# Optimization experiments

Hardware: AMD Instinct MI355X
Metric: run time of the kernel (lower is better)

The kernel has to match this reference:

```python
import jax, jax.numpy as jnp
import numpy as np

HASHMAPS = [(50, 32, 1.0), (200, 16, 0.5), (400, 8, 0.25), (400, 4, 0.125), (400, 3, 0.05)]
CONCAT = 63  # 32+16+8+4+3
PRIMES = jnp.array([73856093, 19349663, 83492791], dtype=jnp.int32)
# corner order idx = i*4 + j*2 + k, bit 0 -> floor, bit 1 -> ceil (matches torch loop)
BITS = jnp.array([[i, j, k] for i in range(2) for j in range(2) for k in range(2)], dtype=jnp.int32)  # (8,3)


def _encode(pos, table, vsl):
    # pos: (N,3) float32; table: (hsize, D)
    p = pos / vsl
    fl = jnp.floor(p)
    fl_i = fl.astype(jnp.int32)
    ce_i = jnp.ceil(p).astype(jnp.int32)
    sel = jnp.where(BITS[None, :, :] == 0, fl_i[:, None, :], ce_i[:, None, :])  # (N,8,3) int32
    sp = sel * PRIMES  # int32 wraparound, same as torch
    h = jnp.mod((sp[..., 0] ^ sp[..., 1]) ^ sp[..., 2], table.shape[0])  # (N,8), nonneg
    emb = table[h]  # (N,8,D) gather
    r = p - fl  # (N,3) trilinear fractions
    # faithful to original: frac weights the FLOOR-corner group (m1/m2/m3 masks)
    lin1 = r[:, 0:1, None] * emb[:, :4] + (1.0 - r[:, 0:1, None]) * emb[:, 4:]   # (N,4,D)
    lin2 = r[:, 1:2, None] * lin1[:, :2] + (1.0 - r[:, 1:2, None]) * lin1[:, 2:]  # (N,2,D)
    lin3 = r[:, 2:3] * lin2[:, 0] + (1.0 - r[:, 2:3]) * lin2[:, 1]               # (N,D)
    return lin3


def setup_inputs() -> dict:
    key = jax.random.key(0)
    ks = jax.random.split(key, 16)
    N = 262144
    inp = {"x": jax.random.normal(ks[0], (N, 3), dtype=jnp.float32)}
    for lvl, (hsize, dim, _) in enumerate(HASHMAPS):
        inp[f"emb{lvl}"] = jax.random.normal(ks[1 + lvl], (hsize, dim), dtype=jnp.float32)
    s = 1.0 / np.sqrt(CONCAT)
    inp["Wd1"] = jax.random.uniform(ks[6], (CONCAT, CONCAT), jnp.float32, -s, s)
    inp["bd1"] = jax.random.uniform(ks[7], (CONCAT,), jnp.float32, -s, s)
    inp["Wd2"] = jax.random.uniform(ks[8], (CONCAT, 1), jnp.float32, -s, s)
    inp["bd2"] = jax.random.uniform(ks[9], (1,), jnp.float32, -s, s)
    inp["Wc1"] = jax.random.uniform(ks[10], (CONCAT, CONCAT), jnp.float32, -s, s)
    inp["bc1"] = jax.random.uniform(ks[11], (CONCAT,), jnp.float32, -s, s)
    inp["Wc2"] = jax.random.uniform(ks[12], (CONCAT, 3), jnp.float32, -s, s)
    inp["bc2"] = jax.random.uniform(ks[13], (3,), jnp.float32, -s, s)
    return inp


def reference(x, emb0, emb1, emb2, emb3, emb4, Wd1, bd1, Wd2, bd2, Wc1, bc1, Wc2, bc2):
    tables = [emb0, emb1, emb2, emb3, emb4]
    feats = [_encode(x, tables[i], HASHMAPS[i][2]) for i in range(5)]
    f = jnp.concatenate(feats, axis=1)  # (N,63)
    dense = jax.nn.relu(f @ Wd1 + bd1) @ Wd2 + bd2  # (N,1)
    color = jax.nn.relu(f @ Wc1 + bc1) @ Wc2 + bc2  # (N,3)
    return (dense, color)
```

## Files before the change

### kernel.cpp

```cpp
#include <hip/hip_runtime.h>
#include <hip/hip_fp16.h>


#define NPTS 262144
#define BLOCK 1024
#define PTS_PER_BLOCK 256

#define IMG_TAB   0
#define IMG_WTF   32768
#define IMG_BW    49152
#define IMG_BYTES 51200

#define OFF_L0 0
#define OFF_L1 2000
#define OFF_L2 6000
#define OFF_L3 10800
#define OFF_L4 12400
#define TAB_HALFS 16384

typedef _Float16 f16x8 __attribute__((ext_vector_type(8)));
typedef _Float16 f16x4 __attribute__((ext_vector_type(4)));
typedef float f32x4 __attribute__((ext_vector_type(4)));

__device__ __forceinline__ void async_cp16(const void* g, void* l) {
    __builtin_amdgcn_global_load_lds(
        (__attribute__((address_space(1))) unsigned int*)const_cast<void*>(g),
        (__attribute__((address_space(3))) unsigned int*)l, 16, 0, 0);
}

__global__ void prep_kernel(const float* __restrict__ Wd1, const float* __restrict__ bd1,
                            const float* __restrict__ Wd2,
                            const float* __restrict__ Wc1, const float* __restrict__ bc1,
                            const float* __restrict__ Wc2,
                            const float* __restrict__ e0, const float* __restrict__ e1,
                            const float* __restrict__ e2, const float* __restrict__ e3,
                            const float* __restrict__ e4,
                            void* __restrict__ ws) {
    _Float16* tab = (_Float16*)((char*)ws + IMG_TAB);
    _Float16* wtf = (_Float16*)((char*)ws + IMG_WTF);
    float*    bw  = (float*)((char*)ws + IMG_BW);
    const int gtid = blockIdx.x * blockDim.x + threadIdx.x;
    const int gstr = gridDim.x * blockDim.x;

    for (int i = gtid; i < 1024; i += gstr) {
        int nt = i >> 7, rem = i & 127, s = rem >> 6, l = rem & 63;
        int kq = l >> 4, lo = l & 15, col = nt * 16 + lo;
#pragma unroll
        for (int j = 0; j < 8; ++j) {
            int k = s * 32 + kq * 8 + j;
            float v = 0.f;
            if (k < 63) {
                if (col < 63) v = Wd1[k * 63 + col];
                else if (col >= 64 && col < 127) v = Wc1[k * 63 + (col - 64)];
            }
            wtf[i * 8 + j] = (_Float16)v;
        }
    }
    for (int i = gtid; i < 512; i += gstr) {
        float v = 0.f;
        if (i < 128) {
            if (i < 63) v = bd1[i];
            else if (i >= 64 && i < 127) v = bc1[i - 64];
        } else if (i < 192) {
            int t = i - 128; v = (t < 63) ? Wd2[t] : 0.f;
        } else if (i < 448) {
            int t = i - 192, c = t >> 2, j = t & 3;
            v = (c < 63 && j < 3) ? Wc2[c * 3 + j] : 0.f;
        }
        bw[i] = v;
    }
    for (int idx = gtid; idx < 50 * 40; idx += gstr) {
        int r = idx / 40, c = idx - r * 40;
        tab[OFF_L0 + idx] = (c < 32) ? (_Float16)e0[r * 32 + c] : (_Float16)0.f;
    }
    for (int idx = gtid; idx < 200 * 20; idx += gstr) {
        int r = idx / 20, c = idx - r * 20;
        tab[OFF_L1 + idx] = (c < 16) ? (_Float16)e1[r * 16 + c] : (_Float16)0.f;
    }
    for (int idx = gtid; idx < 400 * 12; idx += gstr) {
        int r = idx / 12, c = idx - r * 12;
        tab[OFF_L2 + idx] = (c < 8) ? (_Float16)e2[r * 8 + c] : (_Float16)0.f;
    }
    for (int idx = gtid; idx < 400 * 4; idx += gstr)
        tab[OFF_L3 + idx] = (_Float16)e3[idx];
    for (int idx = gtid; idx < 400 * 4; idx += gstr) {
        int r = idx >> 2, c = idx & 3;
        tab[OFF_L4 + idx] = (c < 3) ? (_Float16)e4[r * 3 + c] : (_Float16)0.f;
    }
    for (int idx = 14000 + gtid; idx < TAB_HALFS; idx += gstr)
        tab[idx] = (_Float16)0.f;
}

__device__ __forceinline__ int pymod(int v, int H, int sh) {
    unsigned vu = (unsigned)v ^ 0x80000000u;
    unsigned q = __umulhi(vu >> sh, 0x51EB851Fu) >> 3;
    int m = (int)(vu - q * (unsigned)H);
    int h = m - 48;
    return h < 0 ? h + H : h;
}

struct Corner {
    int ax0, ax1, ay0, ay1, az0, az1;
    float rx, ry, rz;
};
__device__ __forceinline__ Corner mkcorner(float px, float py, float pz) {
    Corner c;
    float fx = floorf(px), fy = floorf(py), fz = floorf(pz);
    c.rx = px - fx; c.ry = py - fy; c.rz = pz - fz;
    c.ax0 = (int)((unsigned)(int)fx * 73856093u);
    c.ax1 = (int)((unsigned)(int)ceilf(px) * 73856093u);
    c.ay0 = (int)((unsigned)(int)fy * 19349663u);
    c.ay1 = (int)((unsigned)(int)ceilf(py) * 19349663u);
    c.az0 = (int)((unsigned)(int)fz * 83492791u);
    c.az1 = (int)((unsigned)(int)ceilf(pz) * 83492791u);
    return c;
}

#define CXOR(C, cc) ((((cc) & 4) ? C.ax1 : C.ax0) ^ (((cc) & 2) ? C.ay1 : C.ay0) \
                   ^ (((cc) & 1) ? C.az1 : C.az0))
#define CW(C, cc) ((((cc) & 4) ? (1.f - C.rx) : C.rx) * \
                   (((cc) & 2) ? (1.f - C.ry) : C.ry) * \
                   (((cc) & 1) ? (1.f - C.rz) : C.rz))

#define ROR_ADD(v, CTRL) { \
    int _t = __builtin_amdgcn_update_dpp(0, __float_as_int(v), (CTRL), 0xF, 0xF, true); \
    (v) += __int_as_float(_t); }
__device__ __forceinline__ float rowsum16(float v) {
    ROR_ADD(v, 0x121)
    ROR_ADD(v, 0x122)
    ROR_ADD(v, 0x124)
    ROR_ADD(v, 0x128)
    return v;
}

__global__ __launch_bounds__(BLOCK, 8) void nerf_fwd(
    const float* __restrict__ x,
    const float* __restrict__ bd2, const float* __restrict__ bc2,
    const void* __restrict__ ws,
    float* __restrict__ out)
{
    __shared__ __align__(16) char ldsb[IMG_BYTES];
    const int tid = threadIdx.x;

    {
        const char* gsrc = (const char*)ws + tid * 16;
        char* ldst = ldsb + tid * 16;
#pragma unroll
        for (int i = 0; i < 3; ++i)
            async_cp16(gsrc + i * 16384, ldst + i * 16384);
        if (tid < 128)
            async_cp16(gsrc + 3 * 16384, ldst + 3 * 16384);
    }

    const int l  = tid & 63;
    const int lo = l & 15;
    const int kq = l >> 4;
    const int wb = blockIdx.x * PTS_PER_BLOCK + (tid >> 6) * 16;
    const int p  = wb + lo;

    const float x0 = x[3 * p + 0], x1 = x[3 * p + 1], x2 = x[3 * p + 2];

    const bool q2 = (kq == 2), q3 = (kq == 3);
    const int  g  = kq >> 1;
    const int  H  = 200 << g;
    const int  sh = 3 + g;
    const float sA = q3 ? 8.f : (q2 ? 4.f : 2.f);
    const int tb0 = q3 ? OFF_L3 : (q2 ? OFF_L2 : OFF_L1);
    const int st  = q3 ? 4 : (q2 ? 12 : 20);
    const int fo0 = (kq == 1) ? 8 : 0;
    const int tb1 = q3 ? OFF_L4 : tb0;
    const int fo1 = q3 ? 0 : fo0 + 4;

    Corner ca = mkcorner(x0, x1, x2);
    Corner cb = mkcorner(x0 * sA, x1 * sA, x2 * sA);
    Corner cb1;
    {
        const float dx = x0 / 0.05f, dy = x1 / 0.05f, dz = x2 / 0.05f;
        const float b1x = q3 ? dx : x0 * sA, b1y = q3 ? dy : x1 * sA,
                    b1z = q3 ? dz : x2 * sA;
        cb1 = mkcorner(b1x, b1y, b1z);
    }
    int hA[8], h0[8], h1[8];
#pragma unroll
    for (int cc = 0; cc < 8; ++cc) hA[cc] = pymod(CXOR(ca, cc), 50, 1);
#pragma unroll
    for (int cc = 0; cc < 8; ++cc) h0[cc] = pymod(CXOR(cb, cc), H, sh);
#pragma unroll
    for (int cc = 0; cc < 8; ++cc) h1[cc] = pymod(CXOR(cb1, cc), H, sh);

    const float bd2v = bd2[0];
    const float bcx = bc2[0], bcy = bc2[1], bcz = bc2[2];

    __syncthreads();

    const _Float16* ldsT = (const _Float16*)ldsb;
    const f16x8* wtf = (const f16x8*)(ldsb + IMG_WTF);
    const float* b1c = (const float*)(ldsb + IMG_BW);
    const float* w2d = b1c + 128;
    const float4* w2c = (const float4*)(b1c + 192);

    const int kq8 = kq * 8;
    f16x8 va[8];
#pragma unroll
    for (int cc = 0; cc < 8; ++cc)
        va[cc] = *(const f16x8*)(ldsT + OFF_L0 + hA[cc] * 40 + kq8);
    f16x4 ea[8];
#pragma unroll
    for (int cc = 0; cc < 8; ++cc)
        ea[cc] = *(const f16x4*)(ldsT + tb0 + h0[cc] * st + fo0);

    float fA[8] = {0.f, 0.f, 0.f, 0.f, 0.f, 0.f, 0.f, 0.f};
#pragma unroll
    for (int cc = 0; cc < 8; ++cc) {
        float w = CW(ca, cc);
#pragma unroll
        for (int j = 0; j < 8; ++j)
            fA[j] = fmaf((float)va[cc][j], w, fA[j]);
    }

    f16x4 eb[8];
#pragma unroll
    for (int cc = 0; cc < 8; ++cc)
        eb[cc] = *(const f16x4*)(ldsT + tb1 + h1[cc] * st + fo1);

    float fB[8] = {0.f, 0.f, 0.f, 0.f, 0.f, 0.f, 0.f, 0.f};
#pragma unroll
    for (int cc = 0; cc < 8; ++cc) {
        float w = CW(cb, cc);
        fB[0] = fmaf((float)ea[cc][0], w, fB[0]); fB[1] = fmaf((float)ea[cc][1], w, fB[1]);
        fB[2] = fmaf((float)ea[cc][2], w, fB[2]); fB[3] = fmaf((float)ea[cc][3], w, fB[3]);
    }
#pragma unroll
    for (int cc = 0; cc < 8; ++cc) {
        float w = CW(cb1, cc);
        fB[4] = fmaf((float)eb[cc][0], w, fB[4]); fB[5] = fmaf((float)eb[cc][1], w, fB[5]);
        fB[6] = fmaf((float)eb[cc][2], w, fB[6]); fB[7] = fmaf((float)eb[cc][3], w, fB[7]);
    }
    if (q3) fB[7] = 0.f;

    union AF { unsigned u[4]; f16x8 h; } a0, a1;
#pragma unroll
    for (int j = 0; j < 4; ++j) {
        __half2 t0 = __floats2half2_rn(fA[2 * j], fA[2 * j + 1]);
        __half2 t1 = __floats2half2_rn(fB[2 * j], fB[2 * j + 1]);
        a0.u[j] = *(unsigned*)&t0;
        a1.u[j] = *(unsigned*)&t1;
    }

    float pd[4]  = {0.f, 0.f, 0.f, 0.f};
    float pc0[4] = {0.f, 0.f, 0.f, 0.f};
    float pc1[4] = {0.f, 0.f, 0.f, 0.f};
    float pc2[4] = {0.f, 0.f, 0.f, 0.f};

#pragma unroll
    for (int nt = 0; nt < 8; ++nt) {
        f16x8 b0 = wtf[(nt * 2 + 0) * 64 + l];
        f16x8 b1 = wtf[(nt * 2 + 1) * 64 + l];
        f32x4 c = {0.f, 0.f, 0.f, 0.f};
        c = __builtin_amdgcn_mfma_f32_16x16x32_f16(a0.h, b0, c, 0, 0, 0);
        c = __builtin_amdgcn_mfma_f32_16x16x32_f16(a1.h, b1, c, 0, 0, 0);
        float bias = b1c[nt * 16 + lo];
        if (nt < 4) {
            float w2 = w2d[nt * 16 + lo];
#pragma unroll
            for (int r = 0; r < 4; ++r)
                pd[r] = fmaf(fmaxf(c[r] + bias, 0.f), w2, pd[r]);
        } else {
            float4 wc = w2c[(nt - 4) * 16 + lo];
#pragma unroll
            for (int r = 0; r < 4; ++r) {
                float t = fmaxf(c[r] + bias, 0.f);
                pc0[r] = fmaf(t, wc.x, pc0[r]);
                pc1[r] = fmaf(t, wc.y, pc1[r]);
                pc2[r] = fmaf(t, wc.z, pc2[r]);
            }
        }
    }

#pragma unroll
    for (int r = 0; r < 4; ++r) {
        pd[r]  = rowsum16(pd[r]);
        pc0[r] = rowsum16(pc0[r]);
        pc1[r] = rowsum16(pc1[r]);
        pc2[r] = rowsum16(pc2[r]);
    }

    if (lo < 4) {
        float badd = (lo == 0) ? bd2v : ((lo == 1) ? bcx : ((lo == 2) ? bcy : bcz));
#pragma unroll
        for (int r = 0; r < 4; ++r) {
            int row = wb + kq * 4 + r;
            int addr = (lo == 0) ? row : (NPTS + row * 3 + (lo - 1));
            float v = (lo == 0) ? pd[r]
                    : ((lo == 1) ? pc0[r] : ((lo == 2) ? pc1[r] : pc2[r]));
            out[addr] = v + badd;
        }
    }
}

extern "C" void kernel_launch(void* const* d_in, const int* in_sizes, int n_in,
                              void* d_out, int out_size, void* d_ws, size_t ws_size,
                              hipStream_t stream) {
    const float* x   = (const float*)d_in[0];
    const float* e0  = (const float*)d_in[1];
    const float* e1  = (const float*)d_in[2];
    const float* e2  = (const float*)d_in[3];
    const float* e3  = (const float*)d_in[4];
    const float* e4  = (const float*)d_in[5];
    const float* Wd1 = (const float*)d_in[6];
    const float* bd1 = (const float*)d_in[7];
    const float* Wd2 = (const float*)d_in[8];
    const float* bd2 = (const float*)d_in[9];
    const float* Wc1 = (const float*)d_in[10];
    const float* bc1 = (const float*)d_in[11];
    const float* Wc2 = (const float*)d_in[12];
    const float* bc2 = (const float*)d_in[13];
    float* out = (float*)d_out;

    prep_kernel<<<64, 256, 0, stream>>>(Wd1, bd1, Wd2, Wc1, bc1, Wc2,
                                        e0, e1, e2, e3, e4, d_ws);
    nerf_fwd<<<dim3(NPTS / PTS_PER_BLOCK), dim3(BLOCK), 0, stream>>>(
        x, bd2, bc2, d_ws, out);
}
```

Measured before the change: 38.00 us.

## Shrink LDS image, halve block size, read bias/W2 from global as float4

```diff
diff --git a/kernel.cpp b/kernel.cpp
--- a/kernel.cpp
+++ b/kernel.cpp
@@ -3,24 +3,26 @@
 
 
 #define NPTS 262144
-#define BLOCK 1024
-#define PTS_PER_BLOCK 256
+#define BLOCK 512
+#define PTS_PER_BLOCK 128
 
 #define IMG_TAB   0
-#define IMG_WTF   32768
-#define IMG_BW    49152
-#define IMG_BYTES 51200
+#define IMG_WTF   24576
+#define IMG_BYTES 40960
+#define IMG_WZ    40960
 
 #define OFF_L0 0
-#define OFF_L1 2000
-#define OFF_L2 6000
-#define OFF_L3 10800
-#define OFF_L4 12400
-#define TAB_HALFS 16384
+#define OFF_L1 1600
+#define OFF_L2 4800
+#define OFF_L3 8000
+#define OFF_L4 9600
+#define TAB_HALFS 12288
 
 typedef _Float16 f16x8 __attribute__((ext_vector_type(8)));
 typedef _Float16 f16x4 __attribute__((ext_vector_type(4)));
 typedef float f32x4 __attribute__((ext_vector_type(4)));
+
+union AF { unsigned u[4]; f16x8 h; };
 
 __device__ __forceinline__ void async_cp16(const void* g, void* l) {
     __builtin_amdgcn_global_load_lds(
@@ -38,7 +40,7 @@
                             void* __restrict__ ws) {
     _Float16* tab = (_Float16*)((char*)ws + IMG_TAB);
     _Float16* wtf = (_Float16*)((char*)ws + IMG_WTF);
-    float*    bw  = (float*)((char*)ws + IMG_BW);
+    float*    bw  = (float*)((char*)ws + IMG_WZ);
     const int gtid = blockIdx.x * blockDim.x + threadIdx.x;
     const int gstr = gridDim.x * blockDim.x;
 
@@ -57,37 +59,32 @@
         }
     }
     for (int i = gtid; i < 512; i += gstr) {
+        int col = i >> 2, j = i & 3;
         float v = 0.f;
-        if (i < 128) {
-            if (i < 63) v = bd1[i];
-            else if (i >= 64 && i < 127) v = bc1[i - 64];
-        } else if (i < 192) {
-            int t = i - 128; v = (t < 63) ? Wd2[t] : 0.f;
-        } else if (i < 448) {
-            int t = i - 192, c = t >> 2, j = t & 3;
-            v = (c < 63 && j < 3) ? Wc2[c * 3 + j] : 0.f;
+        if (j == 0) {
+            if (col < 63) v = bd1[col];
+            else if (col >= 64 && col < 127) v = bc1[col - 64];
+        } else if (col < 64) {
+            if (j == 1 && col < 63) v = Wd2[col];
+        } else {
+            int c2 = col - 64;
+            if (c2 < 63) v = Wc2[c2 * 3 + (j - 1)];
         }
         bw[i] = v;
     }
-    for (int idx = gtid; idx < 50 * 40; idx += gstr) {
-        int r = idx / 40, c = idx - r * 40;
-        tab[OFF_L0 + idx] = (c < 32) ? (_Float16)e0[r * 32 + c] : (_Float16)0.f;
-    }
-    for (int idx = gtid; idx < 200 * 20; idx += gstr) {
-        int r = idx / 20, c = idx - r * 20;
-        tab[OFF_L1 + idx] = (c < 16) ? (_Float16)e1[r * 16 + c] : (_Float16)0.f;
-    }
-    for (int idx = gtid; idx < 400 * 12; idx += gstr) {
-        int r = idx / 12, c = idx - r * 12;
-        tab[OFF_L2 + idx] = (c < 8) ? (_Float16)e2[r * 8 + c] : (_Float16)0.f;
-    }
+    for (int idx = gtid; idx < 50 * 32; idx += gstr)
+        tab[OFF_L0 + idx] = (_Float16)e0[idx];
+    for (int idx = gtid; idx < 200 * 16; idx += gstr)
+        tab[OFF_L1 + idx] = (_Float16)e1[idx];
+    for (int idx = gtid; idx < 400 * 8; idx += gstr)
+        tab[OFF_L2 + idx] = (_Float16)e2[idx];
     for (int idx = gtid; idx < 400 * 4; idx += gstr)
         tab[OFF_L3 + idx] = (_Float16)e3[idx];
     for (int idx = gtid; idx < 400 * 4; idx += gstr) {
         int r = idx >> 2, c = idx & 3;
         tab[OFF_L4 + idx] = (c < 3) ? (_Float16)e4[r * 3 + c] : (_Float16)0.f;
     }
-    for (int idx = 14000 + gtid; idx < TAB_HALFS; idx += gstr)
+    for (int idx = 11200 + gtid; idx < TAB_HALFS; idx += gstr)
         tab[idx] = (_Float16)0.f;
 }
 
@@ -146,10 +143,8 @@
         const char* gsrc = (const char*)ws + tid * 16;
         char* ldst = ldsb + tid * 16;
 #pragma unroll
-        for (int i = 0; i < 3; ++i)
-            async_cp16(gsrc + i * 16384, ldst + i * 16384);
-        if (tid < 128)
-            async_cp16(gsrc + 3 * 16384, ldst + 3 * 16384);
+        for (int i = 0; i < 5; ++i)
+            async_cp16(gsrc + i * 8192, ldst + i * 8192);
     }
 
     const int l  = tid & 63;
@@ -166,7 +161,7 @@
     const int  sh = 3 + g;
     const float sA = q3 ? 8.f : (q2 ? 4.f : 2.f);
     const int tb0 = q3 ? OFF_L3 : (q2 ? OFF_L2 : OFF_L1);
-    const int st  = q3 ? 4 : (q2 ? 12 : 20);
+    const int st  = q3 ? 4 : (q2 ? 8 : 16);
     const int fo0 = (kq == 1) ? 8 : 0;
     const int tb1 = q3 ? OFF_L4 : tb0;
     const int fo1 = q3 ? 0 : fo0 + 4;
@@ -195,15 +190,13 @@
 
     const _Float16* ldsT = (const _Float16*)ldsb;
     const f16x8* wtf = (const f16x8*)(ldsb + IMG_WTF);
-    const float* b1c = (const float*)(ldsb + IMG_BW);
-    const float* w2d = b1c + 128;
-    const float4* w2c = (const float4*)(b1c + 192);
+    const float4* wz = (const float4*)((const char*)ws + IMG_WZ);
 
     const int kq8 = kq * 8;
     f16x8 va[8];
 #pragma unroll
     for (int cc = 0; cc < 8; ++cc)
-        va[cc] = *(const f16x8*)(ldsT + OFF_L0 + hA[cc] * 40 + kq8);
+        va[cc] = *(const f16x8*)(ldsT + OFF_L0 + hA[cc] * 32 + kq8);
     f16x4 ea[8];
 #pragma unroll
     for (int cc = 0; cc < 8; ++cc)
@@ -238,7 +231,7 @@
     }
     if (q3) fB[7] = 0.f;
 
-    union AF { unsigned u[4]; f16x8 h; } a0, a1;
+    AF a0, a1;
 #pragma unroll
     for (int j = 0; j < 4; ++j) {
         __half2 t0 = __floats2half2_rn(fA[2 * j], fA[2 * j + 1]);
@@ -248,9 +241,9 @@
     }
 
     float pd[4]  = {0.f, 0.f, 0.f, 0.f};
-    float pc0[4] = {0.f, 0.f, 0.f, 0.f};
-    float pc1[4] = {0.f, 0.f, 0.f, 0.f};
-    float pc2[4] = {0.f, 0.f, 0.f, 0.f};
+    float px[4]  = {0.f, 0.f, 0.f, 0.f};
+    float py[4]  = {0.f, 0.f, 0.f, 0.f};
+    float pz[4]  = {0.f, 0.f, 0.f, 0.f};
 
 #pragma unroll
     for (int nt = 0; nt < 8; ++nt) {
@@ -259,30 +252,28 @@
         f32x4 c = {0.f, 0.f, 0.f, 0.f};
         c = __builtin_amdgcn_mfma_f32_16x16x32_f16(a0.h, b0, c, 0, 0, 0);
         c = __builtin_amdgcn_mfma_f32_16x16x32_f16(a1.h, b1, c, 0, 0, 0);
-        float bias = b1c[nt * 16 + lo];
+        float4 z = wz[nt * 16 + lo];
         if (nt < 4) {
-            float w2 = w2d[nt * 16 + lo];
 #pragma unroll
             for (int r = 0; r < 4; ++r)
-                pd[r] = fmaf(fmaxf(c[r] + bias, 0.f), w2, pd[r]);
+                pd[r] = fmaf(fmaxf(c[r] + z.x, 0.f), z.y, pd[r]);
         } else {
-            float4 wc = w2c[(nt - 4) * 16 + lo];
 #pragma unroll
             for (int r = 0; r < 4; ++r) {
-                float t = fmaxf(c[r] + bias, 0.f);
-                pc0[r] = fmaf(t, wc.x, pc0[r]);
-                pc1[r] = fmaf(t, wc.y, pc1[r]);
-                pc2[r] = fmaf(t, wc.z, pc2[r]);
+                float t = fmaxf(c[r] + z.x, 0.f);
+                px[r] = fmaf(t, z.y, px[r]);
+                py[r] = fmaf(t, z.z, py[r]);
+                pz[r] = fmaf(t, z.w, pz[r]);
             }
         }
     }
 
 #pragma unroll
     for (int r = 0; r < 4; ++r) {
-        pd[r]  = rowsum16(pd[r]);
-        pc0[r] = rowsum16(pc0[r]);
-        pc1[r] = rowsum16(pc1[r]);
-        pc2[r] = rowsum16(pc2[r]);
+        pd[r] = rowsum16(pd[r]);
+        px[r] = rowsum16(px[r]);
+        py[r] = rowsum16(py[r]);
+        pz[r] = rowsum16(pz[r]);
     }
 
     if (lo < 4) {
@@ -292,7 +283,7 @@
             int row = wb + kq * 4 + r;
             int addr = (lo == 0) ? row : (NPTS + row * 3 + (lo - 1));
             float v = (lo == 0) ? pd[r]
-                    : ((lo == 1) ? pc0[r] : ((lo == 2) ? pc1[r] : pc2[r]));
+                    : ((lo == 1) ? px[r] : ((lo == 2) ? py[r] : pz[r]));
             out[addr] = v + badd;
         }
     }
```

After: 35.92 us. 1.06x faster.
